# Kernel optimization log

Measured on AMD Instinct MI355X. Metric: run time of the kernel, lower is better.

Reference implementation:

```python
import jax, jax.numpy as jnp
import numpy as np

DIM = 768
NUM_HEADS = 12
SMALLEST_RATIO = 0.25
LARGEST_RATIO = 1.0


def setup_inputs() -> dict:
    key = jax.random.key(0)
    k0, k1, k2 = jax.random.split(key, 3)
    B, N = 4, 2048
    x = jax.random.normal(k0, (B, N, DIM), dtype=jnp.float32)
    Wqkv = jax.random.normal(k1, (3 * DIM, DIM), dtype=jnp.float32) * 0.02
    bqkv = jnp.zeros((3 * DIM,), dtype=jnp.float32)
    Wproj = jax.random.normal(k2, (DIM, DIM), dtype=jnp.float32) * 0.02
    bproj = jnp.zeros((DIM,), dtype=jnp.float32)
    return {"x": x, "Wqkv": Wqkv, "bqkv": bqkv, "Wproj": Wproj, "bproj": bproj, "ratio": 1}


def reference(x, Wqkv, bqkv, Wproj, bproj, ratio):
    dc = int(ratio * DIM)
    # dynamic slimmable-width slicing: smallest/largest ratio take leading block,
    # intermediate ratios take trailing block
    if ratio == SMALLEST_RATIO or ratio == LARGEST_RATIO:
        wq, bq = Wqkv[: dc * 3, :dc], bqkv[: dc * 3]
        wp, bp = Wproj[:dc, :dc], bproj[:dc]
    else:
        wq, bq = Wqkv[-dc * 3 :, -dc:], bqkv[-dc * 3 :]
        wp, bp = Wproj[-dc:, -dc:], bproj[-dc:]
    B, N, C = x.shape
    hd = C // NUM_HEADS
    scale = (DIM // NUM_HEADS) ** -0.5  # set at init from full dim, not sliced C
    qkv = x @ wq.T + bq                               # [B, N, 3C]
    qkv = qkv.reshape(B, N, 3, NUM_HEADS, hd).transpose(2, 0, 3, 1, 4)  # [3,B,H,N,hd]
    q, k, v = qkv[0], qkv[1], qkv[2]
    attn = jax.nn.softmax(jnp.einsum("bhqd,bhkd->bhqk", q, k) * scale, axis=-1)
    out = jnp.einsum("bhqk,bhkd->bhqd", attn, v)      # [B,H,N,hd]
    out = out.transpose(0, 2, 1, 3).reshape(B, N, C)
    return out @ wp.T + bp
```

## Files before the change

### kernel.cpp

```cpp
#include <hip/hip_runtime.h>

typedef __bf16 bf16x8 __attribute__((ext_vector_type(8)));
typedef __bf16 bf16x2 __attribute__((ext_vector_type(2)));
typedef float  f32x4  __attribute__((ext_vector_type(4)));
typedef float  f32x16 __attribute__((ext_vector_type(16)));
typedef unsigned short u16;
typedef unsigned u32x2 __attribute__((ext_vector_type(2)));
typedef unsigned u32x4 __attribute__((ext_vector_type(4)));

__device__ __forceinline__ u16 f2bf(float f) {
  return __builtin_bit_cast(u16, (__bf16)f);
}
__device__ __forceinline__ unsigned pack2(float lo, float hi) {
  bf16x2 t;
  t[0] = (__bf16)lo; t[1] = (__bf16)hi;
  return __builtin_bit_cast(unsigned, t);
}

#define GLOAD16(g, l) __builtin_amdgcn_global_load_lds( \
    (__attribute__((address_space(1))) void*)(void*)(g), \
    (__attribute__((address_space(3))) void*)(l), 16, 0, 0)

#define QSCALE 0.18033688011112042f

__global__ __launch_bounds__(256) void cvt_all(
    const float* __restrict__ x, const float* __restrict__ wq,
    const float* __restrict__ wp, unsigned* __restrict__ xb,
    unsigned* __restrict__ wqb, unsigned* __restrict__ wpb) {
  int i = blockIdx.x * 256 + threadIdx.x;
  const float* src;
  unsigned* dst;
  if (i < 786432) {
    src = x; dst = xb;
  } else if (i < 786432 + 221184) {
    src = wq; dst = wqb; i -= 786432;
  } else {
    src = wp; dst = wpb; i -= 786432 + 221184;
  }
  const float4* s = (const float4*)src + 2 * (size_t)i;
  float4 a = s[0], b = s[1];
  u32x4 o = {pack2(a.x, a.y), pack2(a.z, a.w), pack2(b.x, b.y), pack2(b.z, b.w)};
  *((u32x4*)dst + i) = o;
}

template<int EPI, int BK>
__global__ __launch_bounds__(256) void gemm_tn(
    const u16* __restrict__ A, const u16* __restrict__ B,
    const float* __restrict__ bias, float* __restrict__ outF,
    u16* __restrict__ qws, u16* __restrict__ kws, u16* __restrict__ vtws,
    int M, int N, int K) {
  constexpr int TSZ = 128 * BK;
  constexpr int NS = BK / 16;
  __shared__ __align__(16) u16 As[2 * TSZ];
  __shared__ __align__(16) u16 Bs[2 * TSZ];
  const int tid = threadIdx.x;
  const int ln = tid & 63, wv = tid >> 6;
  const int wr = wv >> 1, wc = wv & 1;

  const int flat = (int)(blockIdx.y * gridDim.x + blockIdx.x);
  const int cx = (int)gridDim.x >> 3;
  const int xcd = flat & 7, j = flat >> 3;
  const int bx = xcd * cx + (j % cx);
  const int by = j / cx;
  const int m0 = bx * 128, n0 = by * 128;

  f32x4 acc[4][4] = {};

  const u16* ag[NS];
  const u16* bg[NS];
#pragma unroll
  for (int u = 0; u < NS; ++u) {
    int s = tid + u * 256;
    int h = s >> 9, sr = (s & 511) >> 2;
    int kc = ((s & 3) ^ ((sr >> 1) & 3)) * 8 + h * 32;
    ag[u] = A + (size_t)(m0 + sr) * K + kc;
    bg[u] = B + (size_t)(n0 + sr) * K + kc;
  }

#pragma unroll
  for (int u = 0; u < NS; ++u) {
    GLOAD16(ag[u], As + u * 2048 + wv * 512);
    GLOAD16(bg[u], Bs + u * 2048 + wv * 512);
  }
  __syncthreads();

  int cur = 0;
  for (int k0 = 0; k0 < K; k0 += BK) {
    const int nxt = cur ^ 1;
    if (k0 + BK < K) {
#pragma unroll
      for (int u = 0; u < NS; ++u) {
        GLOAD16(ag[u] + k0 + BK, As + nxt * TSZ + u * 2048 + wv * 512);
        GLOAD16(bg[u] + k0 + BK, Bs + nxt * TSZ + u * 2048 + wv * 512);
      }
    }
#pragma unroll
    for (int ks = 0; ks < BK / 32; ++ks) {
      const u16* ab = As + cur * TSZ + ks * 4096;
      const u16* bb = Bs + cur * TSZ + ks * 4096;
      bf16x8 af[4], bfr[4];
#pragma unroll
      for (int i = 0; i < 4; ++i) {
        int ra = wr * 64 + i * 16 + (ln & 15);
        af[i] = *(const bf16x8*)(ab + ra * 32 + (((ln >> 4) ^ ((ra >> 1) & 3)) * 8));
        int rb = wc * 64 + i * 16 + (ln & 15);
        bfr[i] = *(const bf16x8*)(bb + rb * 32 + (((ln >> 4) ^ ((rb >> 1) & 3)) * 8));
      }
#pragma unroll
      for (int i = 0; i < 4; ++i)
#pragma unroll
        for (int j2 = 0; j2 < 4; ++j2)
          acc[i][j2] = __builtin_amdgcn_mfma_f32_16x16x32_bf16(af[i], bfr[j2], acc[i][j2], 0, 0, 0);
    }
    __syncthreads();
    cur = nxt;
  }

  if (EPI == 1) {
#pragma unroll
    for (int j2 = 0; j2 < 4; ++j2) {
      int col = n0 + wc * 64 + j2 * 16 + (ln & 15);
      float bj = bias[col];
#pragma unroll
      for (int i = 0; i < 4; ++i) {
        int mr = m0 + wr * 64 + i * 16 + ((ln >> 4) << 2);
#pragma unroll
        for (int r = 0; r < 4; ++r)
          outF[(size_t)(mr + r) * N + col] = acc[i][j2][r] + bj;
      }
    }
  } else {
    const int s = n0 / 768;
#pragma unroll
    for (int j2 = 0; j2 < 4; ++j2) {
      int col = n0 + wc * 64 + j2 * 16 + (ln & 15);
      float bj = bias[col];
      int ns = col - s * 768;
      int h = ns >> 6, d = ns & 63;
#pragma unroll
      for (int i = 0; i < 4; ++i) {
        int m = m0 + wr * 64 + i * 16 + ((ln >> 4) << 2);
        int b = m >> 11, iseq = m & 2047;
        size_t bh = (size_t)(b * 12 + h);
        if (s == 0) {
#pragma unroll
          for (int r = 0; r < 4; ++r)
            qws[(bh * 2048 + iseq + r) * 64 + d] = f2bf((acc[i][j2][r] + bj) * QSCALE);
        } else if (s == 1) {
#pragma unroll
          for (int r = 0; r < 4; ++r)
            kws[(bh * 2048 + iseq + r) * 64 + d] = f2bf(acc[i][j2][r] + bj);
        } else {
          u32x2 pk = {pack2(acc[i][j2][0] + bj, acc[i][j2][1] + bj),
                      pack2(acc[i][j2][2] + bj, acc[i][j2][3] + bj)};
          *(u32x2*)(vtws + ((size_t)bh * 64 + (iseq >> 5)) * 2048 +
                    ((iseq >> 3) & 3) * 512 + (size_t)d * 8 + (iseq & 7)) = pk;
        }
      }
    }
  }
}

#define SWZ(v) (((v) & 32) | (((v) & 31) ^ (ln & 31)))
__global__ __launch_bounds__(256, 3) void attn_fa(
    const u16* __restrict__ qws, const u16* __restrict__ kws,
    const u16* __restrict__ vtws, u16* __restrict__ aows) {
  __shared__ __align__(16) u16 SM[16384];
  __shared__ float Ls[256];
  const int tid = threadIdx.x, ln = tid & 63, wv = tid >> 6;
  const int lq = ln & 31, hi = ln >> 5;
  const int qw = wv & 1;
  const int p  = wv >> 1;

  const int flat = blockIdx.y * 16 + blockIdx.x;
  const int xcd = flat & 7, jj = flat >> 3;
  const int bh = xcd * 6 + (jj % 6);
  const int q0 = (jj / 6) * 128 + qw * 64;

  const int kv0 = p * 1024;
  const size_t kbase = (size_t)bh * 2048 * 64;

  bf16x8 qf[2][4];
#pragma unroll
  for (int g = 0; g < 2; ++g) {
    const u16* qp = qws + kbase + (size_t)(q0 + g * 32 + lq) * 64 + hi * 8;
#pragma unroll
    for (int dc = 0; dc < 4; ++dc) qf[g][dc] = *(const bf16x8*)(qp + dc * 16);
  }

  const f32x16 zc = {};
  f32x16 o0[2] = {}, o1[2] = {};
  float lsum[2] = {0.f, 0.f};

  int koff[4], voff[2];
#pragma unroll
  for (int dc = 0; dc < 4; ++dc)
    koff[dc] = lq * 64 + (((dc * 2 + hi) ^ (lq & 7)) * 8);
#pragma unroll
  for (int c = 0; c < 2; ++c)
    voff[c] = (c * 2 + hi) * 512 + lq * 8;

  const int s0i = qw * 128 + ln, s1i = s0i + 64;
  const int kvA = s0i >> 3, kvB = s1i >> 3;
  const int piA = (kvA & ~12) | ((kvA & 4) << 1) | ((kvA & 8) >> 1);
  const int piB = (kvB & ~12) | ((kvB & 4) << 1) | ((kvB & 8) >> 1);
  const u16* kg0 = kws + kbase + (size_t)(kv0 + piA) * 64 + (((s0i & 7) ^ (kvA & 7)) * 8);
  const u16* kg1 = kws + kbase + (size_t)(kv0 + piB) * 64 + (((s1i & 7) ^ (kvB & 7)) * 8);
  const u16* vg  = vtws + ((size_t)bh * 64 + (kv0 >> 5)) * 2048 + s0i * 8;
  u16* Kb = SM + p * 4096;
  u16* Vb = SM + 8192 + p * 4096;
  const int sd = qw * 1024;

#define STAGE(buf, t) do { \
    GLOAD16(kg0 + (size_t)(t) * 2048, Kb + (buf) * 2048 + sd); \
    GLOAD16(kg1 + (size_t)(t) * 2048, Kb + (buf) * 2048 + sd + 512); \
    GLOAD16(vg + (size_t)(t) * 2048, Vb + (buf) * 2048 + sd); \
    GLOAD16(vg + (size_t)(t) * 2048 + 512, Vb + (buf) * 2048 + sd + 512); \
  } while (0)

  STAGE(0, 0);
  __syncthreads();

  int cur = 0;
  for (int it = 0; it < 32; ++it) {
    const int nxt = cur ^ 1;
    if (it + 1 < 32) STAGE(nxt, it + 1);
    const u16* kbuf = Kb + cur * 2048;
    const u16* vbuf = Vb + cur * 2048;

    f32x16 s[2];
    {
      bf16x8 kf = *(const bf16x8*)(kbuf + koff[0]);
      s[0] = __builtin_amdgcn_mfma_f32_32x32x16_bf16(kf, qf[0][0], zc, 0, 0, 0);
      s[1] = __builtin_amdgcn_mfma_f32_32x32x16_bf16(kf, qf[1][0], zc, 0, 0, 0);
    }
#pragma unroll
    for (int dc = 1; dc < 4; ++dc) {
      bf16x8 kf = *(const bf16x8*)(kbuf + koff[dc]);
      s[0] = __builtin_amdgcn_mfma_f32_32x32x16_bf16(kf, qf[0][dc], s[0], 0, 0, 0);
      s[1] = __builtin_amdgcn_mfma_f32_32x32x16_bf16(kf, qf[1][dc], s[1], 0, 0, 0);
    }

#pragma unroll
    for (int g = 0; g < 2; ++g) {
      float a = 0.f;
#pragma unroll
      for (int r = 0; r < 16; ++r) {
        float e = __builtin_amdgcn_exp2f(s[g][r]); s[g][r] = e; a += e;
      }
      lsum[g] += a;
    }

#pragma unroll
    for (int c = 0; c < 2; ++c) {
      bf16x8 va = *(const bf16x8*)(vbuf + voff[c]);
      bf16x8 vb2 = *(const bf16x8*)(vbuf + voff[c] + 256);
#pragma unroll
      for (int g = 0; g < 2; ++g) {
        const int base = c * 8;
        u32x4 pw = {pack2(s[g][base + 0], s[g][base + 1]),
                    pack2(s[g][base + 2], s[g][base + 3]),
                    pack2(s[g][base + 4], s[g][base + 5]),
                    pack2(s[g][base + 6], s[g][base + 7])};
        bf16x8 pfrag = __builtin_bit_cast(bf16x8, pw);
        o0[g] = __builtin_amdgcn_mfma_f32_32x32x16_bf16(va, pfrag, o0[g], 0, 0, 0);
        o1[g] = __builtin_amdgcn_mfma_f32_32x32x16_bf16(vb2, pfrag, o1[g], 0, 0, 0);
      }
    }
    __syncthreads();
    cur = nxt;
  }
#undef STAGE

  float lg[2];
#pragma unroll
  for (int g = 0; g < 2; ++g) {
    lg[g] = lsum[g];
    lg[g] += __shfl_xor(lg[g], 32);
  }

  float* exO = (float*)SM + qw * 4096 + ln * 64;
  if (p == 1) {
#pragma unroll
    for (int r = 0; r < 16; ++r) {
      exO[SWZ(r)]      = o0[0][r];
      exO[SWZ(16 + r)] = o1[0][r];
      exO[SWZ(32 + r)] = o0[1][r];
      exO[SWZ(48 + r)] = o1[1][r];
    }
    Ls[qw * 128 + ln * 2 + 0] = lg[0];
    Ls[qw * 128 + ln * 2 + 1] = lg[1];
  }
  __syncthreads();
  if (p == 0) {
#pragma unroll
    for (int r = 0; r < 16; ++r) {
      o0[0][r] += exO[SWZ(r)];
      o1[0][r] += exO[SWZ(16 + r)];
      o0[1][r] += exO[SWZ(32 + r)];
      o1[1][r] += exO[SWZ(48 + r)];
    }
    lg[0] += Ls[qw * 128 + ln * 2 + 0];
    lg[1] += Ls[qw * 128 + ln * 2 + 1];

    const int b = bh / 12, h = bh % 12;
#pragma unroll
    for (int g = 0; g < 2; ++g) {
      const float rl = 1.0f / lg[g];
      u16* orow = aows + (size_t)(b * 2048 + q0 + g * 32 + lq) * 768 + h * 64;
#pragma unroll
      for (int t = 0; t < 4; ++t) {
        u32x2 pk0 = {pack2(o0[g][4 * t + 0] * rl, o0[g][4 * t + 1] * rl),
                     pack2(o0[g][4 * t + 2] * rl, o0[g][4 * t + 3] * rl)};
        u32x2 pk1 = {pack2(o1[g][4 * t + 0] * rl, o1[g][4 * t + 1] * rl),
                     pack2(o1[g][4 * t + 2] * rl, o1[g][4 * t + 3] * rl)};
        *(u32x2*)(orow + t * 8 + 4 * hi)      = pk0;
        *(u32x2*)(orow + 32 + t * 8 + 4 * hi) = pk1;
      }
    }
  }
}

extern "C" void kernel_launch(void* const* d_in, const int* in_sizes, int n_in,
                              void* d_out, int out_size, void* d_ws, size_t ws_size,
                              hipStream_t stream) {
  const float* x     = (const float*)d_in[0];
  const float* Wqkv  = (const float*)d_in[1];
  const float* bqkv  = (const float*)d_in[2];
  const float* Wproj = (const float*)d_in[3];
  const float* bproj = (const float*)d_in[4];
  float* out = (float*)d_out;

  u16* xb   = (u16*)d_ws;
  u16* wqb  = xb  + 6291456;
  u16* wpb  = wqb + 1769472;
  u16* qws  = wpb + 589824;
  u16* kws  = qws + 6291456;
  u16* vtws = kws + 6291456;
  u16* aows = vtws + 6291456;

  cvt_all<<<4224, 256, 0, stream>>>(x, Wqkv, Wproj,
                                    (unsigned*)xb, (unsigned*)wqb, (unsigned*)wpb);

  gemm_tn<0, 32><<<dim3(64, 18), 256, 0, stream>>>(xb, wqb, bqkv, nullptr,
                                                   qws, kws, vtws, 8192, 2304, 768);
  attn_fa<<<dim3(16, 48), 256, 0, stream>>>(qws, kws, vtws, aows);
  gemm_tn<1, 64><<<dim3(64, 6), 256, 0, stream>>>(aows, wpb, bproj, out,
                                                  nullptr, nullptr, nullptr,
                                                  8192, 768, 768);
}
```

Before: 134.3 us.

## Fuse fp32-to-bf16 conversion of x into the QKV GEMM A-tile load

```diff
diff --git a/kernel.cpp b/kernel.cpp
--- a/kernel.cpp
+++ b/kernel.cpp
@@ -23,19 +23,16 @@
 
 #define QSCALE 0.18033688011112042f
 
-__global__ __launch_bounds__(256) void cvt_all(
-    const float* __restrict__ x, const float* __restrict__ wq,
-    const float* __restrict__ wp, unsigned* __restrict__ xb,
+__global__ __launch_bounds__(256) void cvt_w(
+    const float* __restrict__ wq, const float* __restrict__ wp,
     unsigned* __restrict__ wqb, unsigned* __restrict__ wpb) {
   int i = blockIdx.x * 256 + threadIdx.x;
   const float* src;
   unsigned* dst;
-  if (i < 786432) {
-    src = x; dst = xb;
-  } else if (i < 786432 + 221184) {
-    src = wq; dst = wqb; i -= 786432;
+  if (i < 221184) {
+    src = wq; dst = wqb;
   } else {
-    src = wp; dst = wpb; i -= 786432 + 221184;
+    src = wp; dst = wpb; i -= 221184;
   }
   const float4* s = (const float4*)src + 2 * (size_t)i;
   float4 a = s[0], b = s[1];
@@ -43,15 +40,17 @@
   *((u32x4*)dst + i) = o;
 }
 
-template<int EPI, int BK>
+template<int EPI, int BK, int AF32>
 __global__ __launch_bounds__(256) void gemm_tn(
-    const u16* __restrict__ A, const u16* __restrict__ B,
+    const u16* __restrict__ Au, const u16* __restrict__ B,
     const float* __restrict__ bias, float* __restrict__ outF,
     u16* __restrict__ qws, u16* __restrict__ kws, u16* __restrict__ vtws,
     int M, int N, int K) {
-  constexpr int TSZ = 128 * BK;
-  constexpr int NS = BK / 16;
-  __shared__ __align__(16) u16 As[2 * TSZ];
+  constexpr int TSZ  = 128 * BK;
+  constexpr int ATSZ = AF32 ? 2 * TSZ : TSZ;
+  constexpr int NS   = BK / 16;
+  constexpr int NSA  = AF32 ? BK / 8 : BK / 16;
+  __shared__ __align__(16) u16 As[2 * ATSZ];
   __shared__ __align__(16) u16 Bs[2 * TSZ];
   const int tid = threadIdx.x;
   const int ln = tid & 63, wv = tid >> 6;
@@ -64,45 +63,84 @@
   const int by = j / cx;
   const int m0 = bx * 128, n0 = by * 128;
 
+  const float* Af = (const float*)Au;
+
   f32x4 acc[4][4] = {};
 
-  const u16* ag[NS];
   const u16* bg[NS];
 #pragma unroll
   for (int u = 0; u < NS; ++u) {
     int s = tid + u * 256;
     int h = s >> 9, sr = (s & 511) >> 2;
     int kc = ((s & 3) ^ ((sr >> 1) & 3)) * 8 + h * 32;
-    ag[u] = A + (size_t)(m0 + sr) * K + kc;
     bg[u] = B + (size_t)(n0 + sr) * K + kc;
   }
-
-#pragma unroll
-  for (int u = 0; u < NS; ++u) {
-    GLOAD16(ag[u], As + u * 2048 + wv * 512);
-    GLOAD16(bg[u], Bs + u * 2048 + wv * 512);
-  }
+  const u16* agb[NS];
+  const float* agf[NSA];
+  if constexpr (AF32) {
+#pragma unroll
+    for (int u = 0; u < NSA; ++u) {
+      int s = tid + u * 256;
+      int r = s >> 3;
+      int c = (s & 7) ^ (r & 7);
+      agf[u] = Af + (size_t)(m0 + r) * K + c * 4;
+    }
+  } else {
+#pragma unroll
+    for (int u = 0; u < NS; ++u) {
+      int s = tid + u * 256;
+      int h = s >> 9, sr = (s & 511) >> 2;
+      int kc = ((s & 3) ^ ((sr >> 1) & 3)) * 8 + h * 32;
+      agb[u] = Au + (size_t)(m0 + sr) * K + kc;
+    }
+  }
+
+  if constexpr (AF32) {
+#pragma unroll
+    for (int u = 0; u < NSA; ++u) GLOAD16(agf[u], As + u * 2048 + wv * 512);
+  } else {
+#pragma unroll
+    for (int u = 0; u < NS; ++u) GLOAD16(agb[u], As + u * 2048 + wv * 512);
+  }
+#pragma unroll
+  for (int u = 0; u < NS; ++u) GLOAD16(bg[u], Bs + u * 2048 + wv * 512);
   __syncthreads();
 
   int cur = 0;
   for (int k0 = 0; k0 < K; k0 += BK) {
     const int nxt = cur ^ 1;
     if (k0 + BK < K) {
-#pragma unroll
-      for (int u = 0; u < NS; ++u) {
-        GLOAD16(ag[u] + k0 + BK, As + nxt * TSZ + u * 2048 + wv * 512);
+      if constexpr (AF32) {
+#pragma unroll
+        for (int u = 0; u < NSA; ++u)
+          GLOAD16(agf[u] + k0 + BK, As + nxt * ATSZ + u * 2048 + wv * 512);
+      } else {
+#pragma unroll
+        for (int u = 0; u < NS; ++u)
+          GLOAD16(agb[u] + k0 + BK, As + nxt * ATSZ + u * 2048 + wv * 512);
+      }
+#pragma unroll
+      for (int u = 0; u < NS; ++u)
         GLOAD16(bg[u] + k0 + BK, Bs + nxt * TSZ + u * 2048 + wv * 512);
-      }
     }
 #pragma unroll
     for (int ks = 0; ks < BK / 32; ++ks) {
-      const u16* ab = As + cur * TSZ + ks * 4096;
+      const u16* ab = As + cur * ATSZ + ks * (AF32 ? 8192 : 4096);
       const u16* bb = Bs + cur * TSZ + ks * 4096;
       bf16x8 af[4], bfr[4];
 #pragma unroll
       for (int i = 0; i < 4; ++i) {
         int ra = wr * 64 + i * 16 + (ln & 15);
-        af[i] = *(const bf16x8*)(ab + ra * 32 + (((ln >> 4) ^ ((ra >> 1) & 3)) * 8));
+        if constexpr (AF32) {
+          int x7 = ra & 7, c2 = (ln >> 4) * 2;
+          float4 lo = *(const float4*)(ab + (size_t)ra * 64 + ((c2 ^ x7) * 8));
+          float4 hi = *(const float4*)(ab + (size_t)ra * 64 + (((c2 + 1) ^ x7) * 8));
+          u32x4 aw = {pack2(lo.x, lo.y), pack2(lo.z, lo.w),
+                      pack2(hi.x, hi.y), pack2(hi.z, hi.w)};
+          af[i] = __builtin_bit_cast(bf16x8, aw);
+        } else {
+          af[i] = *(const bf16x8*)(ab + ra * 32 + (((ln >> 4) ^ ((ra >> 1) & 3)) * 8));
+        }
         int rb = wc * 64 + i * 16 + (ln & 15);
         bfr[i] = *(const bf16x8*)(bb + rb * 32 + (((ln >> 4) ^ ((rb >> 1) & 3)) * 8));
       }
@@ -339,13 +377,13 @@
   u16* vtws = kws + 6291456;
   u16* aows = vtws + 6291456;
 
-  cvt_all<<<4224, 256, 0, stream>>>(x, Wqkv, Wproj,
-                                    (unsigned*)xb, (unsigned*)wqb, (unsigned*)wpb);
-
-  gemm_tn<0, 32><<<dim3(64, 18), 256, 0, stream>>>(xb, wqb, bqkv, nullptr,
-                                                   qws, kws, vtws, 8192, 2304, 768);
+  cvt_w<<<1152, 256, 0, stream>>>(Wqkv, Wproj, (unsigned*)wqb, (unsigned*)wpb);
+
+  gemm_tn<0, 32, 1><<<dim3(64, 18), 256, 0, stream>>>((const u16*)x, wqb, bqkv,
+                                                      nullptr, qws, kws, vtws,
+                                                      8192, 2304, 768);
   attn_fa<<<dim3(16, 48), 256, 0, stream>>>(qws, kws, vtws, aows);
-  gemm_tn<1, 64><<<dim3(64, 6), 256, 0, stream>>>(aows, wpb, bproj, out,
-                                                  nullptr, nullptr, nullptr,
-                                                  8192, 768, 768);
-}
+  gemm_tn<1, 64, 0><<<dim3(64, 6), 256, 0, stream>>>(aows, wpb, bproj, out,
+                                                     nullptr, nullptr, nullptr,
+                                                     8192, 768, 768);
+}
```

New measurement: 140.8 us. +4.8%, slower.
